# Kernel optimization log

Hardware: AMD Instinct MI355X
Metric: run time of the kernel (lower is better)

The kernel has to match this reference:

```python
import jax, jax.numpy as jnp
import numpy as np

# dims: B batch, T seq, DM d_model, H kv heads, D head dim
B, T, DM = 4, 2048, 768
H, D = 4, 64          # n_kv_heads, d_head = d_model // n_heads = 768 // 12
DIM = H * D           # 256


def setup_inputs() -> dict:
    key = jax.random.key(0)
    kx, kq, kk, kv, ko, kg = jax.random.split(key, 6)
    s = 0.02  # init scale for weights
    return {
        "x": jax.random.normal(kx, (B, T, DM), jnp.float32),
        "Wq": jax.random.normal(kq, (DM, DIM), jnp.float32) * s,
        "Wk": jax.random.normal(kk, (DM, DIM), jnp.float32) * s,
        "Wv": jax.random.normal(kv, (DM, DIM), jnp.float32) * s,
        "Wo": jax.random.normal(ko, (DIM, DM), jnp.float32) * s,
        "Wg": jax.random.normal(kg, (DM, DM), jnp.float32) * s,
    }


def _feature_map(x):
    # F.elu(x) + 1.0  (strictly positive features)
    return jax.nn.elu(x) + 1.0


def reference(x, Wq, Wk, Wv, Wo, Wg):
    Bx, Tx, _ = x.shape
    q = _feature_map((x @ Wq).reshape(Bx, Tx, H, D))
    k = _feature_map((x @ Wk).reshape(Bx, Tx, H, D))
    v = (x @ Wv).reshape(Bx, Tx, H, D)

    # time-major for scan: [T, B, H, D]
    qT = q.transpose(1, 0, 2, 3)
    kT = k.transpose(1, 0, 2, 3)
    vT = v.transpose(1, 0, 2, 3)

    S0 = jnp.zeros((Bx, H, D, D), x.dtype)  # running sum of k v^T
    z0 = jnp.zeros((Bx, H, D), x.dtype)     # running sum of k

    def step(carry, inp):
        S, z = carry
        qi, ki, vi = inp  # each [B, H, D]
        S = S + ki[..., :, None] * vi[..., None, :]   # outer product update
        z = z + ki
        num = jnp.einsum('bhd,bhde->bhe', qi, S)
        den = jnp.maximum(jnp.sum(qi * z, axis=-1), 1e-6)  # clamp(min=1e-6)
        return (S, z), num / den[..., None]

    (_, _), outT = jax.lax.scan(step, (S0, z0), (qT, kT, vT))

    out = outT.transpose(1, 0, 2, 3).reshape(Bx, Tx, DIM)  # [B, T, H*D]
    gate = jax.nn.sigmoid(x @ Wg)
    return (out @ Wo) * gate
```

## Files before the change

kernel.cpp:

```cpp
#include <hip/hip_runtime.h>
#include <math.h>

typedef __attribute__((ext_vector_type(8))) short bf16x8;
typedef __attribute__((ext_vector_type(4))) float f32x4;

namespace {
constexpr int Bb  = 4;
constexpr int Tt  = 2048;
constexpr int DM  = 768;
constexpr int Hh  = 4;
constexpr int Dd  = 64;
constexpr int DIM = 256;
constexpr int BT  = Bb * Tt;
constexpr int CH  = 64;
constexpr int NC  = Tt / CH;
constexpr int NQKVG = 1536;
constexpr int MT  = BT / 128;
}

__device__ __forceinline__ float elu1(float x) { return x > 0.f ? x + 1.f : expf(x); }

__device__ __forceinline__ unsigned short f2bf(float f) {
  unsigned int x = __float_as_uint(f);
  unsigned int r = (x + 0x7fffu + ((x >> 16) & 1u)) >> 16;
  return (unsigned short)r;
}
__device__ __forceinline__ float bf2f(unsigned short u) {
  return __uint_as_float((unsigned int)u << 16);
}

__device__ __forceinline__ void gload16(const void* g, void* l) {
  __builtin_amdgcn_global_load_lds(
      (const __attribute__((address_space(1))) void*)g,
      (__attribute__((address_space(3))) void*)l, 16, 0, 0);
}

struct Stage32 {
  const short* a[2];
  const short* b[2];
  int seg;
  __device__ __forceinline__ void init(const short* Ag, size_t lda,
                                       const short* Bg, size_t ldb, int w, int l) {
    const int c16 = (l & 3) ^ ((l >> 3) & 3);
    seg = w * 2;
#pragma unroll
    for (int j = 0; j < 2; ++j) {
      int row = (seg + j) * 16 + (l >> 2);
      a[j] = Ag + (size_t)row * lda + c16 * 8;
      b[j] = Bg + (size_t)row * ldb + c16 * 8;
    }
  }
  __device__ __forceinline__ void issue(int k0, short* as, short* bs) const {
#pragma unroll
    for (int j = 0; j < 2; ++j) {
      gload16(a[j] + k0, (char*)as + (seg + j) * 1024);
      gload16(b[j] + k0, (char*)bs + (seg + j) * 1024);
    }
  }
};

__device__ __forceinline__ void xcd_tile(int bid, int& mt, int& nt) {
  int xcd = bid & 7;
  int idx = bid >> 3;
  mt = xcd * 8 + (idx & 7);
  nt = idx >> 3;
}

template <int NT>
__device__ __forceinline__ void kloop32(const Stage32& st, short* As0, short* As1,
                                        short* Bs0, short* Bs1,
                                        f32x4 (&acc)[4][4], int wr, int wc,
                                        int lr, int lg) {
  st.issue(0, As0, Bs0);
  st.issue(32, As1, Bs1);
#pragma unroll
  for (int t = 0; t < NT; ++t) {
    short* as = (t & 1) ? As1 : As0;
    short* bs = (t & 1) ? Bs1 : Bs0;
    if (t + 1 < NT)
      asm volatile("s_waitcnt vmcnt(4)" ::: "memory");
    else
      asm volatile("s_waitcnt vmcnt(0)" ::: "memory");
    __builtin_amdgcn_s_barrier();
    bf16x8 af[4], bf[4];
#pragma unroll
    for (int mi = 0; mi < 4; ++mi) {
      int r = wr * 64 + mi * 16 + lr;
      af[mi] = *(const bf16x8*)&as[r * 32 + (lg ^ ((r >> 1) & 3)) * 8];
    }
#pragma unroll
    for (int ni = 0; ni < 4; ++ni) {
      int r = wc * 64 + ni * 16 + lr;
      bf[ni] = *(const bf16x8*)&bs[r * 32 + (lg ^ ((r >> 1) & 3)) * 8];
    }
    asm volatile("s_waitcnt lgkmcnt(0)" ::: "memory");
    __builtin_amdgcn_sched_barrier(0);
    __builtin_amdgcn_s_barrier();
    if (t + 2 < NT) st.issue((t + 2) * 32, as, bs);
    __builtin_amdgcn_s_setprio(1);
#pragma unroll
    for (int mi = 0; mi < 4; ++mi)
#pragma unroll
      for (int ni = 0; ni < 4; ++ni)
        acc[mi][ni] = __builtin_amdgcn_mfma_f32_16x16x32_bf16(
            af[mi], bf[ni], acc[mi][ni], 0, 0, 0);
    __builtin_amdgcn_s_setprio(0);
  }
}

__global__ __launch_bounds__(256) void k_prep(
    const float* __restrict__ x, const float* __restrict__ Wq,
    const float* __restrict__ Wk, const float* __restrict__ Wv,
    const float* __restrict__ Wg, const float* __restrict__ Wo,
    unsigned short* __restrict__ xb, unsigned short* __restrict__ WT,
    unsigned short* __restrict__ WoT) {
  int bid = blockIdx.x;
  if (bid < 3072) {
    int i = bid * 256 + threadIdx.x;
    const float4* p = (const float4*)(x + (size_t)i * 8);
    float4 a = p[0], b = p[1];
    union { unsigned short u[8]; uint4 v; } r;
    r.u[0] = f2bf(a.x); r.u[1] = f2bf(a.y); r.u[2] = f2bf(a.z); r.u[3] = f2bf(a.w);
    r.u[4] = f2bf(b.x); r.u[5] = f2bf(b.y); r.u[6] = f2bf(b.z); r.u[7] = f2bf(b.w);
    *(uint4*)(xb + (size_t)i * 8) = r.v;
    return;
  }
  __shared__ float t[32][33];
  int idx = bid - 3072;
  const float* src;
  unsigned short* out;
  int K, N, n_off, ldo;
  if (idx < 576) {
    int z = idx / 192;
    idx %= 192;
    src = (z == 0) ? Wq : (z == 1) ? Wk : Wv;
    out = WT; K = 768; N = 256; n_off = z * 256; ldo = 768;
  } else if (idx < 1152) {
    idx -= 576;
    src = Wg; out = WT; K = 768; N = 768; n_off = 768; ldo = 768;
  } else {
    idx -= 1152;
    src = Wo; out = WoT; K = 256; N = 768; n_off = 0; ldo = 256;
  }
  int kt = idx % (K / 32), nt = idx / (K / 32);
  int k0 = kt * 32, n0 = nt * 32;
  const int tx = threadIdx.x & 31, ty = threadIdx.x >> 5;
  for (int i = ty; i < 32; i += 8)
    t[i][tx] = src[(size_t)(k0 + i) * N + n0 + tx];
  __syncthreads();
  for (int i = ty; i < 32; i += 8)
    out[(size_t)(n_off + n0 + i) * ldo + k0 + tx] = f2bf(t[tx][i]);
}

__global__ __launch_bounds__(256, 4) void k_gemm1(
    const unsigned short* __restrict__ xb, const unsigned short* __restrict__ WT,
    unsigned short* __restrict__ Q, unsigned short* __restrict__ K,
    unsigned short* __restrict__ V, unsigned short* __restrict__ G) {
  __shared__ __align__(16) char smem[32768];
  short* As0 = (short*)smem;
  short* As1 = (short*)(smem + 8192);
  short* Bs0 = (short*)(smem + 16384);
  short* Bs1 = (short*)(smem + 24576);
  const int tid = threadIdx.x;
  const int w = tid >> 6, l = tid & 63;
  const int lr = l & 15, lg = l >> 4;
  const int wr = w >> 1, wc = w & 1;
  int mt, nt;
  xcd_tile(blockIdx.x, mt, nt);
  const int m0 = mt * 128, n0 = nt * 128;

  Stage32 st;
  st.init((const short*)xb + (size_t)m0 * DM, DM,
          (const short*)WT + (size_t)n0 * DM, DM, w, l);

  f32x4 acc[4][4];
#pragma unroll
  for (int i = 0; i < 4; ++i)
#pragma unroll
    for (int j = 0; j < 4; ++j) acc[i][j] = (f32x4){0.f, 0.f, 0.f, 0.f};

  kloop32<DM / 32>(st, As0, As1, Bs0, Bs1, acc, wr, wc, lr, lg);
  __syncthreads();

  const int ttype = (n0 < 512) ? 0 : (n0 < 768) ? 1 : 2;
  unsigned short* Cs = (unsigned short*)smem;
#pragma unroll
  for (int mi = 0; mi < 4; ++mi)
#pragma unroll
    for (int ni = 0; ni < 4; ++ni)
#pragma unroll
      for (int r = 0; r < 4; ++r) {
        float v = acc[mi][ni][r];
        if (ttype == 0) v = elu1(v);
        else if (ttype == 2) v = 1.f / (1.f + expf(-v));
        Cs[(wr * 64 + mi * 16 + lg * 4 + r) * 128 + wc * 64 + ni * 16 + lr] =
            f2bf(v);
      }
  __syncthreads();
  unsigned short* dst;
  int ldd, cb;
  if (n0 < 256)      { dst = Q; ldd = DIM; cb = n0; }
  else if (n0 < 512) { dst = K; ldd = DIM; cb = n0 - 256; }
  else if (n0 < 768) { dst = V; ldd = DIM; cb = n0 - 512; }
  else               { dst = G; ldd = DM;  cb = n0 - 768; }
  const uint4* Cv = (const uint4*)Cs;
#pragma unroll
  for (int i = 0; i < 8; ++i) {
    int idx = tid + i * 256;
    int urow = idx >> 4, uc = idx & 15;
    *(uint4*)(dst + (size_t)(m0 + urow) * ldd + cb + uc * 8) = Cv[idx];
  }
}

__global__ __launch_bounds__(256) void k_chunksum(
    const unsigned short* __restrict__ K, const unsigned short* __restrict__ V,
    float* __restrict__ Sc, float* __restrict__ zc) {
  __shared__ __align__(16) char smem[16384];
  short* Kt = (short*)smem;
  short* Vt = (short*)(smem + 8192);
  const int c = blockIdx.x, h = blockIdx.y, b = blockIdx.z;
  const int tid = threadIdx.x;
  const int w = tid >> 6, l = tid & 63;
  const int lr = l & 15, lg = l >> 4;
  const size_t rowbase = ((size_t)(b * Tt + c * CH)) * DIM + h * Dd;

#pragma unroll
  for (int it = 0; it < 4; ++it) {
    int idx = tid + it * 256;
    int t = idx >> 4, d4 = idx & 15;
    short4 k4 = *(const short4*)((const short*)K + rowbase + (size_t)t * DIM + d4 * 4);
    short4 v4 = *(const short4*)((const short*)V + rowbase + (size_t)t * DIM + d4 * 4);
    const short* kk = (const short*)&k4;
    const short* vv = (const short*)&v4;
#pragma unroll
    for (int j = 0; j < 4; ++j) {
      int e = d4 * 4 + j;
      int sl = ((t >> 3) ^ (e & 7)) * 16 + (t & 7) * 2;
      *(short*)((char*)Kt + e * 128 + sl) = kk[j];
      *(short*)((char*)Vt + e * 128 + sl) = vv[j];
    }
  }
  __syncthreads();

  if (tid < Dd) {
    float s = 0.f;
    for (int t = 0; t < CH; ++t) {
      unsigned short u = *(const unsigned short*)(
          (char*)Kt + tid * 128 + (((t >> 3) ^ (tid & 7)) * 16) + (t & 7) * 2);
      s += bf2f(u);
    }
    zc[((size_t)(b * Hh + h) * NC + c) * Dd + tid] = s;
  }

  f32x4 a[4];
#pragma unroll
  for (int nf = 0; nf < 4; ++nf) a[nf] = (f32x4){0.f, 0.f, 0.f, 0.f};
  const int rd = w * 16 + lr;
#pragma unroll
  for (int ks = 0; ks < 2; ++ks) {
    bf16x8 af = *(const bf16x8*)((char*)Kt + rd * 128 +
                                 (((ks * 4 + lg) ^ (rd & 7)) * 16));
#pragma unroll
    for (int nf = 0; nf < 4; ++nf) {
      int re = nf * 16 + lr;
      bf16x8 bf = *(const bf16x8*)((char*)Vt + re * 128 +
                                   (((ks * 4 + lg) ^ (re & 7)) * 16));
      a[nf] = __builtin_amdgcn_mfma_f32_16x16x32_bf16(af, bf, a[nf], 0, 0, 0);
    }
  }
  __syncthreads();

  float* Cf = (float*)smem;
#pragma unroll
  for (int nf = 0; nf < 4; ++nf)
#pragma unroll
    for (int r = 0; r < 4; ++r)
      Cf[(w * 16 + lg * 4 + r) * 64 + nf * 16 + lr] = a[nf][r];
  __syncthreads();
  const size_t base = ((size_t)(b * Hh + h) * NC + c) * (Dd * Dd);
  const float4* Cv = (const float4*)Cf;
#pragma unroll
  for (int it = 0; it < 4; ++it) {
    int idx = tid + it * 256;
    *(float4*)&Sc[base + (size_t)idx * 4] = Cv[idx];
  }
}

__global__ __launch_bounds__(256) void k_scan(float* __restrict__ Sc,
                                              float* __restrict__ zc) {
  const int bh = blockIdx.x;
  const int o = blockIdx.y * 256 + threadIdx.x;
  const size_t base = (size_t)bh * NC * (Dd * Dd) + o;
  float v[NC];
#pragma unroll
  for (int c = 0; c < NC; ++c) v[c] = Sc[base + (size_t)c * (Dd * Dd)];
  float run = 0.f;
#pragma unroll
  for (int c = 0; c < NC; ++c) {
    Sc[base + (size_t)c * (Dd * Dd)] = run;
    run += v[c];
  }
  if (blockIdx.y == 0 && threadIdx.x < Dd) {
    float rz = 0.f;
    for (int c = 0; c < NC; ++c) {
      size_t oz = ((size_t)bh * NC + c) * Dd + threadIdx.x;
      float cur = zc[oz];
      zc[oz] = rz;
      rz += cur;
    }
  }
}

__global__ __launch_bounds__(256) void k_out(
    const unsigned short* __restrict__ Q, const unsigned short* __restrict__ K,
    const unsigned short* __restrict__ V, const float* __restrict__ Sc,
    const float* __restrict__ zc, unsigned short* __restrict__ O) {
  __shared__ __align__(16) char smem[41216];
  short* Qs = (short*)smem;
  short* Ks = (short*)(smem + 8192);
  short* Vt = (short*)(smem + 16384);
  short* St = (short*)(smem + 24576);
  short* Ps = (short*)(smem + 32768);
  float* zs = (float*)(smem + 40960);
  const int c = blockIdx.x, h = blockIdx.y, b = blockIdx.z;
  const int tid = threadIdx.x;
  const int w = tid >> 6, l = tid & 63;
  const int lr = l & 15, lg = l >> 4;
  const size_t rowbase = ((size_t)(b * Tt + c * CH)) * DIM + h * Dd;

  {
    const int c16 = (l & 7) ^ ((l >> 3) & 7);
#pragma unroll
    for (int i = 0; i < 2; ++i) {
      int row = i * 32 + w * 8 + (l >> 3);
      gload16((const short*)Q + rowbase + (size_t)row * DIM + c16 * 8,
              (char*)Qs + (i * 32 + w * 8) * 128);
      gload16((const short*)K + rowbase + (size_t)row * DIM + c16 * 8,
              (char*)Ks + (i * 32 + w * 8) * 128);
    }
  }
  const size_t sbase = ((size_t)(b * Hh + h) * NC + c) * (Dd * Dd);
  if (tid < Dd) zs[tid] = zc[((size_t)(b * Hh + h) * NC + c) * Dd + tid];
#pragma unroll
  for (int it = 0; it < 4; ++it) {
    int idx = tid + it * 256;
    int t = idx >> 4, d4 = idx & 15;
    short4 v4 = *(const short4*)((const short*)V + rowbase + (size_t)t * DIM + d4 * 4);
    const short* vv = (const short*)&v4;
#pragma unroll
    for (int j = 0; j < 4; ++j) {
      int e = d4 * 4 + j;
      *(short*)((char*)Vt + e * 128 + (((t >> 3) ^ (e & 7)) * 16) + (t & 7) * 2) = vv[j];
    }
    float4 s4 = *(const float4*)&Sc[sbase + (size_t)t * 64 + d4 * 4];
    const float* sv = (const float*)&s4;
#pragma unroll
    for (int j = 0; j < 4; ++j) {
      int e = d4 * 4 + j;
      *(short*)((char*)St + e * 128 + (((t >> 3) ^ (e & 7)) * 16) + (t & 7) * 2) =
          (short)f2bf(sv[j]);
    }
  }
  __syncthreads();

  f32x4 a0[4];
#pragma unroll
  for (int nf = 0; nf < 4; ++nf) a0[nf] = (f32x4){0.f, 0.f, 0.f, 0.f};
  const int rq = w * 16 + lr;
#pragma unroll
  for (int ks = 0; ks < 2; ++ks) {
    bf16x8 af = *(const bf16x8*)((char*)Qs + rq * 128 +
                                 (((ks * 4 + lg) ^ (rq & 7)) * 16));
#pragma unroll
    for (int nf = 0; nf < 4; ++nf) {
      int rk = nf * 16 + lr;
      bf16x8 bf = *(const bf16x8*)((char*)Ks + rk * 128 +
                                   (((ks * 4 + lg) ^ (rk & 7)) * 16));
      a0[nf] = __builtin_amdgcn_mfma_f32_16x16x32_bf16(af, bf, a0[nf], 0, 0, 0);
    }
  }

  float part[4] = {0.f, 0.f, 0.f, 0.f};
#pragma unroll
  for (int nf = 0; nf < 4; ++nf) {
    int col = nf * 16 + lr;
#pragma unroll
    for (int r = 0; r < 4; ++r) {
      int row = w * 16 + lg * 4 + r;
      float av = (col <= row) ? a0[nf][r] : 0.f;
      part[r] += av;
      *(short*)((char*)Ps + row * 128 +
                ((((nf * 2) + (lr >> 3)) ^ (row & 7)) * 16) + (lr & 7) * 2) =
          (short)f2bf(av);
    }
  }
#pragma unroll
  for (int r = 0; r < 4; ++r) {
    int row = w * 16 + lg * 4 + r;
#pragma unroll
    for (int j = 0; j < 4; ++j) {
      int d = lr + j * 16;
      unsigned short qu = *(const unsigned short*)(
          (char*)Qs + row * 128 + (((d >> 3) ^ (row & 7)) * 16) + (d & 7) * 2);
      part[r] += bf2f(qu) * zs[d];
    }
  }
  float inv[4];
#pragma unroll
  for (int r = 0; r < 4; ++r) {
    float s = part[r];
    s += __shfl_xor(s, 1);
    s += __shfl_xor(s, 2);
    s += __shfl_xor(s, 4);
    s += __shfl_xor(s, 8);
    inv[r] = 1.f / fmaxf(s, 1e-6f);
  }
  __syncthreads();

  f32x4 a1[4];
#pragma unroll
  for (int nf = 0; nf < 4; ++nf) a1[nf] = (f32x4){0.f, 0.f, 0.f, 0.f};
#pragma unroll
  for (int ks = 0; ks < 4; ++ks) {
    const char* abase = (ks < 2) ? (const char*)Ps : (const char*)Qs;
    const char* bbase = (ks < 2) ? (const char*)Vt : (const char*)St;
    int kslot = (ks & 1) * 4 + lg;
    bf16x8 af = *(const bf16x8*)(abase + rq * 128 + ((kslot ^ (rq & 7)) * 16));
#pragma unroll
    for (int nf = 0; nf < 4; ++nf) {
      int re = nf * 16 + lr;
      bf16x8 bf = *(const bf16x8*)(bbase + re * 128 + ((kslot ^ (re & 7)) * 16));
      a1[nf] = __builtin_amdgcn_mfma_f32_16x16x32_bf16(af, bf, a1[nf], 0, 0, 0);
    }
  }
  __syncthreads();

#pragma unroll
  for (int nf = 0; nf < 4; ++nf)
#pragma unroll
    for (int r = 0; r < 4; ++r) {
      int row = w * 16 + lg * 4 + r;
      Ps[row * 64 + nf * 16 + lr] = (short)f2bf(a1[nf][r] * inv[r]);
    }
  __syncthreads();
  const uint4* Pv = (const uint4*)Ps;
#pragma unroll
  for (int i = 0; i < 2; ++i) {
    int idx = tid + i * 256;
    int row = idx >> 3, uc = idx & 7;
    *(uint4*)((unsigned short*)O + rowbase + (size_t)row * DIM + uc * 8) = Pv[idx];
  }
}

__global__ __launch_bounds__(256, 4) void k_gemm2(
    const unsigned short* __restrict__ Ob, const unsigned short* __restrict__ WoT,
    const unsigned short* __restrict__ G, float* __restrict__ out) {
  __shared__ __align__(16) char smem[32768];
  short* As0 = (short*)smem;
  short* As1 = (short*)(smem + 8192);
  short* Bs0 = (short*)(smem + 16384);
  short* Bs1 = (short*)(smem + 24576);
  const int tid = threadIdx.x;
  const int w = tid >> 6, l = tid & 63;
  const int lr = l & 15, lg = l >> 4;
  const int wr = w >> 1, wc = w & 1;
  int mt, nt;
  xcd_tile(blockIdx.x, mt, nt);
  const int m0 = mt * 128, n0 = nt * 128;

  Stage32 st;
  st.init((const short*)Ob + (size_t)m0 * DIM, DIM,
          (const short*)WoT + (size_t)n0 * DIM, DIM, w, l);

  f32x4 acc[4][4];
#pragma unroll
  for (int i = 0; i < 4; ++i)
#pragma unroll
    for (int j = 0; j < 4; ++j) acc[i][j] = (f32x4){0.f, 0.f, 0.f, 0.f};

  kloop32<DIM / 32>(st, As0, As1, Bs0, Bs1, acc, wr, wc, lr, lg);

  float* Cf = (float*)smem;
#pragma unroll
  for (int half = 0; half < 2; ++half) {
    __syncthreads();
    if (wr == half) {
#pragma unroll
      for (int mi = 0; mi < 4; ++mi)
#pragma unroll
        for (int ni = 0; ni < 4; ++ni)
#pragma unroll
          for (int r = 0; r < 4; ++r)
            Cf[(mi * 16 + lg * 4 + r) * 128 + wc * 64 + ni * 16 + lr] =
                acc[mi][ni][r];
    }
    __syncthreads();
    const float4* Cv = (const float4*)Cf;
#pragma unroll
    for (int i = 0; i < 8; ++i) {
      int idx = tid + i * 256;
      int urow = idx >> 5, uc = idx & 31;
      float4 cv = Cv[idx];
      size_t go = (size_t)(m0 + half * 64 + urow) * DM + n0 + uc * 4;
      short4 g4 = *(const short4*)(G + go);
      float4 ov;
      ov.x = cv.x * bf2f(g4.x);
      ov.y = cv.y * bf2f(g4.y);
      ov.z = cv.z * bf2f(g4.z);
      ov.w = cv.w * bf2f(g4.w);
      *(float4*)(out + go) = ov;
    }
  }
}

extern "C" void kernel_launch(void* const* d_in, const int* in_sizes, int n_in,
                              void* d_out, int out_size, void* d_ws,
                              size_t ws_size, hipStream_t stream) {
  const float* x  = (const float*)d_in[0];
  const float* Wq = (const float*)d_in[1];
  const float* Wk = (const float*)d_in[2];
  const float* Wv = (const float*)d_in[3];
  const float* Wo = (const float*)d_in[4];
  const float* Wg = (const float*)d_in[5];
  float* out = (float*)d_out;

  char* p = (char*)d_ws;
  size_t off = 0;
  auto alloc = [&](size_t bytes) {
    void* r = p + off;
    off = (off + bytes + 255) & ~(size_t)255;
    return r;
  };
  unsigned short* xb  = (unsigned short*)alloc((size_t)BT * DM * 2);
  unsigned short* WT  = (unsigned short*)alloc((size_t)NQKVG * DM * 2);
  unsigned short* WoT = (unsigned short*)alloc((size_t)DM * DIM * 2);
  unsigned short* Q   = (unsigned short*)alloc((size_t)BT * DIM * 2);
  unsigned short* Kf  = (unsigned short*)alloc((size_t)BT * DIM * 2);
  unsigned short* Vf  = (unsigned short*)alloc((size_t)BT * DIM * 2);
  unsigned short* G   = (unsigned short*)alloc((size_t)BT * DM * 2);
  unsigned short* Ob  = (unsigned short*)alloc((size_t)BT * DIM * 2);
  float* Sc = (float*)alloc((size_t)Bb * Hh * NC * Dd * Dd * 4);
  float* zc = (float*)alloc((size_t)Bb * Hh * NC * Dd * 4);

  k_prep<<<dim3(3072 + 1344), dim3(256), 0, stream>>>(x, Wq, Wk, Wv, Wg, Wo,
                                                      xb, WT, WoT);

  k_gemm1<<<dim3(MT * (NQKVG / 128)), dim3(256), 0, stream>>>(
      xb, WT, Q, Kf, Vf, G);

  k_chunksum<<<dim3(NC, Hh, Bb), dim3(256), 0, stream>>>(Kf, Vf, Sc, zc);
  k_scan<<<dim3(Bb * Hh, Dd * Dd / 256), dim3(256), 0, stream>>>(Sc, zc);
  k_out<<<dim3(NC, Hh, Bb), dim3(256), 0, stream>>>(Q, Kf, Vf, Sc, zc, Ob);

  k_gemm2<<<dim3(MT * (DM / 128)), dim3(256), 0, stream>>>(Ob, WoT, G, out);
}
```

Baseline: 76.95 us.

## Widen GEMM tiles to 128x256 for projection and output GEMMs

Both bf16 MFMA GEMMs move from 128x128 to 128x256 output tiles. Each warp now computes a 64x128 sub-tile with 32 accumulators, and the B-operand staging and LDS buffers grow to match. The aim is better operand reuse per loaded A tile and fewer blocks. In exchange, register pressure roughly doubles (launch bounds drop to 2 blocks per CU), and grid sizes halve (gemm1 goes to 384 blocks, gemm2 to 192), which may underfill 256 CUs. The epilogues are split into column halves and quarters to fit the shared scratch buffer.

```diff
diff --git a/kernel.cpp b/kernel.cpp
--- a/kernel.cpp
+++ b/kernel.cpp
@@ -35,27 +35,33 @@
       (__attribute__((address_space(3))) void*)l, 16, 0, 0);
 }
 
-struct Stage32 {
+struct StageW {
   const short* a[2];
-  const short* b[2];
-  int seg;
+  const short* b[4];
+  int sega, segb;
   __device__ __forceinline__ void init(const short* Ag, size_t lda,
                                        const short* Bg, size_t ldb, int w, int l) {
     const int c16 = (l & 3) ^ ((l >> 3) & 3);
-    seg = w * 2;
+    sega = w * 2;
+    segb = w * 4;
 #pragma unroll
     for (int j = 0; j < 2; ++j) {
-      int row = (seg + j) * 16 + (l >> 2);
+      int row = (sega + j) * 16 + (l >> 2);
       a[j] = Ag + (size_t)row * lda + c16 * 8;
+    }
+#pragma unroll
+    for (int j = 0; j < 4; ++j) {
+      int row = (segb + j) * 16 + (l >> 2);
       b[j] = Bg + (size_t)row * ldb + c16 * 8;
     }
   }
   __device__ __forceinline__ void issue(int k0, short* as, short* bs) const {
 #pragma unroll
-    for (int j = 0; j < 2; ++j) {
-      gload16(a[j] + k0, (char*)as + (seg + j) * 1024);
-      gload16(b[j] + k0, (char*)bs + (seg + j) * 1024);
-    }
+    for (int j = 0; j < 2; ++j)
+      gload16(a[j] + k0, (char*)as + (sega + j) * 1024);
+#pragma unroll
+    for (int j = 0; j < 4; ++j)
+      gload16(b[j] + k0, (char*)bs + (segb + j) * 1024);
   }
 };
 
@@ -67,10 +73,10 @@
 }
 
 template <int NT>
-__device__ __forceinline__ void kloop32(const Stage32& st, short* As0, short* As1,
-                                        short* Bs0, short* Bs1,
-                                        f32x4 (&acc)[4][4], int wr, int wc,
-                                        int lr, int lg) {
+__device__ __forceinline__ void kloopW(const StageW& st, short* As0, short* As1,
+                                       short* Bs0, short* Bs1,
+                                       f32x4 (&acc)[4][8], int wr, int wc,
+                                       int lr, int lg) {
   st.issue(0, As0, Bs0);
   st.issue(32, As1, Bs1);
 #pragma unroll
@@ -78,19 +84,19 @@
     short* as = (t & 1) ? As1 : As0;
     short* bs = (t & 1) ? Bs1 : Bs0;
     if (t + 1 < NT)
-      asm volatile("s_waitcnt vmcnt(4)" ::: "memory");
+      asm volatile("s_waitcnt vmcnt(6)" ::: "memory");
     else
       asm volatile("s_waitcnt vmcnt(0)" ::: "memory");
     __builtin_amdgcn_s_barrier();
-    bf16x8 af[4], bf[4];
+    bf16x8 af[4], bf[8];
 #pragma unroll
     for (int mi = 0; mi < 4; ++mi) {
       int r = wr * 64 + mi * 16 + lr;
       af[mi] = *(const bf16x8*)&as[r * 32 + (lg ^ ((r >> 1) & 3)) * 8];
     }
 #pragma unroll
-    for (int ni = 0; ni < 4; ++ni) {
-      int r = wc * 64 + ni * 16 + lr;
+    for (int ni = 0; ni < 8; ++ni) {
+      int r = wc * 128 + ni * 16 + lr;
       bf[ni] = *(const bf16x8*)&bs[r * 32 + (lg ^ ((r >> 1) & 3)) * 8];
     }
     asm volatile("s_waitcnt lgkmcnt(0)" ::: "memory");
@@ -101,7 +107,7 @@
 #pragma unroll
     for (int mi = 0; mi < 4; ++mi)
 #pragma unroll
-      for (int ni = 0; ni < 4; ++ni)
+      for (int ni = 0; ni < 8; ++ni)
         acc[mi][ni] = __builtin_amdgcn_mfma_f32_16x16x32_bf16(
             af[mi], bf[ni], acc[mi][ni], 0, 0, 0);
     __builtin_amdgcn_s_setprio(0);
@@ -152,63 +158,68 @@
     out[(size_t)(n_off + n0 + i) * ldo + k0 + tx] = f2bf(t[tx][i]);
 }
 
-__global__ __launch_bounds__(256, 4) void k_gemm1(
+__global__ __launch_bounds__(256, 2) void k_gemm1(
     const unsigned short* __restrict__ xb, const unsigned short* __restrict__ WT,
     unsigned short* __restrict__ Q, unsigned short* __restrict__ K,
     unsigned short* __restrict__ V, unsigned short* __restrict__ G) {
-  __shared__ __align__(16) char smem[32768];
+  __shared__ __align__(16) char smem[49152];
   short* As0 = (short*)smem;
   short* As1 = (short*)(smem + 8192);
   short* Bs0 = (short*)(smem + 16384);
-  short* Bs1 = (short*)(smem + 24576);
+  short* Bs1 = (short*)(smem + 32768);
   const int tid = threadIdx.x;
   const int w = tid >> 6, l = tid & 63;
   const int lr = l & 15, lg = l >> 4;
   const int wr = w >> 1, wc = w & 1;
   int mt, nt;
   xcd_tile(blockIdx.x, mt, nt);
-  const int m0 = mt * 128, n0 = nt * 128;
-
-  Stage32 st;
+  const int m0 = mt * 128, n0 = nt * 256;
+
+  StageW st;
   st.init((const short*)xb + (size_t)m0 * DM, DM,
           (const short*)WT + (size_t)n0 * DM, DM, w, l);
 
-  f32x4 acc[4][4];
+  f32x4 acc[4][8];
 #pragma unroll
   for (int i = 0; i < 4; ++i)
 #pragma unroll
-    for (int j = 0; j < 4; ++j) acc[i][j] = (f32x4){0.f, 0.f, 0.f, 0.f};
-
-  kloop32<DM / 32>(st, As0, As1, Bs0, Bs1, acc, wr, wc, lr, lg);
-  __syncthreads();
+    for (int j = 0; j < 8; ++j) acc[i][j] = (f32x4){0.f, 0.f, 0.f, 0.f};
+
+  kloopW<DM / 32>(st, As0, As1, Bs0, Bs1, acc, wr, wc, lr, lg);
 
   const int ttype = (n0 < 512) ? 0 : (n0 < 768) ? 1 : 2;
-  unsigned short* Cs = (unsigned short*)smem;
-#pragma unroll
-  for (int mi = 0; mi < 4; ++mi)
-#pragma unroll
-    for (int ni = 0; ni < 4; ++ni)
-#pragma unroll
-      for (int r = 0; r < 4; ++r) {
-        float v = acc[mi][ni][r];
-        if (ttype == 0) v = elu1(v);
-        else if (ttype == 2) v = 1.f / (1.f + expf(-v));
-        Cs[(wr * 64 + mi * 16 + lg * 4 + r) * 128 + wc * 64 + ni * 16 + lr] =
-            f2bf(v);
-      }
-  __syncthreads();
   unsigned short* dst;
   int ldd, cb;
-  if (n0 < 256)      { dst = Q; ldd = DIM; cb = n0; }
-  else if (n0 < 512) { dst = K; ldd = DIM; cb = n0 - 256; }
-  else if (n0 < 768) { dst = V; ldd = DIM; cb = n0 - 512; }
+  if (n0 < 256)      { dst = Q; ldd = DIM; cb = 0; }
+  else if (n0 < 512) { dst = K; ldd = DIM; cb = 0; }
+  else if (n0 < 768) { dst = V; ldd = DIM; cb = 0; }
   else               { dst = G; ldd = DM;  cb = n0 - 768; }
-  const uint4* Cv = (const uint4*)Cs;
-#pragma unroll
-  for (int i = 0; i < 8; ++i) {
-    int idx = tid + i * 256;
-    int urow = idx >> 4, uc = idx & 15;
-    *(uint4*)(dst + (size_t)(m0 + urow) * ldd + cb + uc * 8) = Cv[idx];
+  unsigned short* Cs = (unsigned short*)smem;
+#pragma unroll
+  for (int hc = 0; hc < 2; ++hc) {
+    __syncthreads();
+    if (wc == hc) {
+#pragma unroll
+      for (int mi = 0; mi < 4; ++mi)
+#pragma unroll
+        for (int ni = 0; ni < 8; ++ni)
+#pragma unroll
+          for (int r = 0; r < 4; ++r) {
+            float v = acc[mi][ni][r];
+            if (ttype == 0) v = elu1(v);
+            else if (ttype == 2) v = 1.f / (1.f + expf(-v));
+            Cs[(wr * 64 + mi * 16 + lg * 4 + r) * 128 + ni * 16 + lr] = f2bf(v);
+          }
+    }
+    __syncthreads();
+    const uint4* Cv = (const uint4*)Cs;
+#pragma unroll
+    for (int i = 0; i < 8; ++i) {
+      int idx = tid + i * 256;
+      int urow = idx >> 4, uc = idx & 15;
+      *(uint4*)(dst + (size_t)(m0 + urow) * ldd + cb + hc * 128 + uc * 8) =
+          Cv[idx];
+    }
   }
 }
 
@@ -452,65 +463,66 @@
   }
 }
 
-__global__ __launch_bounds__(256, 4) void k_gemm2(
+__global__ __launch_bounds__(256, 2) void k_gemm2(
     const unsigned short* __restrict__ Ob, const unsigned short* __restrict__ WoT,
     const unsigned short* __restrict__ G, float* __restrict__ out) {
-  __shared__ __align__(16) char smem[32768];
+  __shared__ __align__(16) char smem[49152];
   short* As0 = (short*)smem;
   short* As1 = (short*)(smem + 8192);
   short* Bs0 = (short*)(smem + 16384);
-  short* Bs1 = (short*)(smem + 24576);
+  short* Bs1 = (short*)(smem + 32768);
   const int tid = threadIdx.x;
   const int w = tid >> 6, l = tid & 63;
   const int lr = l & 15, lg = l >> 4;
   const int wr = w >> 1, wc = w & 1;
   int mt, nt;
   xcd_tile(blockIdx.x, mt, nt);
-  const int m0 = mt * 128, n0 = nt * 128;
-
-  Stage32 st;
+  const int m0 = mt * 128, n0 = nt * 256;
+
+  StageW st;
   st.init((const short*)Ob + (size_t)m0 * DIM, DIM,
           (const short*)WoT + (size_t)n0 * DIM, DIM, w, l);
 
-  f32x4 acc[4][4];
+  f32x4 acc[4][8];
 #pragma unroll
   for (int i = 0; i < 4; ++i)
 #pragma unroll
-    for (int j = 0; j < 4; ++j) acc[i][j] = (f32x4){0.f, 0.f, 0.f, 0.f};
-
-  kloop32<DIM / 32>(st, As0, As1, Bs0, Bs1, acc, wr, wc, lr, lg);
+    for (int j = 0; j < 8; ++j) acc[i][j] = (f32x4){0.f, 0.f, 0.f, 0.f};
+
+  kloopW<DIM / 32>(st, As0, As1, Bs0, Bs1, acc, wr, wc, lr, lg);
 
   float* Cf = (float*)smem;
 #pragma unroll
-  for (int half = 0; half < 2; ++half) {
-    __syncthreads();
-    if (wr == half) {
-#pragma unroll
-      for (int mi = 0; mi < 4; ++mi)
-#pragma unroll
-        for (int ni = 0; ni < 4; ++ni)
-#pragma unroll
-          for (int r = 0; r < 4; ++r)
-            Cf[(mi * 16 + lg * 4 + r) * 128 + wc * 64 + ni * 16 + lr] =
-                acc[mi][ni][r];
-    }
-    __syncthreads();
-    const float4* Cv = (const float4*)Cf;
-#pragma unroll
-    for (int i = 0; i < 8; ++i) {
-      int idx = tid + i * 256;
-      int urow = idx >> 5, uc = idx & 31;
-      float4 cv = Cv[idx];
-      size_t go = (size_t)(m0 + half * 64 + urow) * DM + n0 + uc * 4;
-      short4 g4 = *(const short4*)(G + go);
-      float4 ov;
-      ov.x = cv.x * bf2f(g4.x);
-      ov.y = cv.y * bf2f(g4.y);
-      ov.z = cv.z * bf2f(g4.z);
-      ov.w = cv.w * bf2f(g4.w);
-      *(float4*)(out + go) = ov;
-    }
-  }
+  for (int qr = 0; qr < 2; ++qr)
+#pragma unroll
+    for (int qc = 0; qc < 2; ++qc) {
+      __syncthreads();
+      if (wr == qr && wc == qc) {
+#pragma unroll
+        for (int mi = 0; mi < 4; ++mi)
+#pragma unroll
+          for (int ni = 0; ni < 8; ++ni)
+#pragma unroll
+            for (int r = 0; r < 4; ++r)
+              Cf[(mi * 16 + lg * 4 + r) * 128 + ni * 16 + lr] = acc[mi][ni][r];
+      }
+      __syncthreads();
+      const float4* Cv = (const float4*)Cf;
+#pragma unroll
+      for (int i = 0; i < 8; ++i) {
+        int idx = tid + i * 256;
+        int urow = idx >> 5, uc = idx & 31;
+        float4 cv = Cv[idx];
+        size_t go = (size_t)(m0 + qr * 64 + urow) * DM + n0 + qc * 128 + uc * 4;
+        short4 g4 = *(const short4*)(G + go);
+        float4 ov;
+        ov.x = cv.x * bf2f(g4.x);
+        ov.y = cv.y * bf2f(g4.y);
+        ov.z = cv.z * bf2f(g4.z);
+        ov.w = cv.w * bf2f(g4.w);
+        *(float4*)(out + go) = ov;
+      }
+    }
 }
 
 extern "C" void kernel_launch(void* const* d_in, const int* in_sizes, int n_in,
@@ -545,12 +557,12 @@
   k_prep<<<dim3(3072 + 1344), dim3(256), 0, stream>>>(x, Wq, Wk, Wv, Wg, Wo,
                                                       xb, WT, WoT);
 
-  k_gemm1<<<dim3(MT * (NQKVG / 128)), dim3(256), 0, stream>>>(
+  k_gemm1<<<dim3(MT * (NQKVG / 256)), dim3(256), 0, stream>>>(
       xb, WT, Q, Kf, Vf, G);
 
   k_chunksum<<<dim3(NC, Hh, Bb), dim3(256), 0, stream>>>(Kf, Vf, Sc, zc);
   k_scan<<<dim3(Bb * Hh, Dd * Dd / 256), dim3(256), 0, stream>>>(Sc, zc);
   k_out<<<dim3(NC, Hh, Bb), dim3(256), 0, stream>>>(Q, Kf, Vf, Sc, zc, Ob);
 
-  k_gemm2<<<dim3(MT * (DM / 128)), dim3(256), 0, stream>>>(Ob, WoT, G, out);
-}
+  k_gemm2<<<dim3(MT * (DM / 256)), dim3(256), 0, stream>>>(Ob, WoT, G, out);
+}
```

After: 95.76 us. +24.4%, slower.

## Triple-buffer GEMM k-loop and store chunk state sums in bf16

Applied to the files above, without the earlier changes.

The GEMM main loop moves from two LDS stages to three. This lets the prefetch for stage t+2 be issued right after the first barrier, and the second per-iteration barrier is removed. LDS per block grows to 48KB and launch bounds drop to 3 blocks per CU. Separately, the per-chunk KV state sums are stored and scanned in bf16 instead of fp32, which halves the traffic through chunksum, scan and out. The cost is extra rounding in the prefix sums, which are carried in fp32 but written back as bf16. The scan also no longer preloads all chunks into registers.

```diff
diff --git a/kernel.cpp b/kernel.cpp
--- a/kernel.cpp
+++ b/kernel.cpp
@@ -67,21 +67,27 @@
 }
 
 template <int NT>
-__device__ __forceinline__ void kloop32(const Stage32& st, short* As0, short* As1,
-                                        short* Bs0, short* Bs1,
-                                        f32x4 (&acc)[4][4], int wr, int wc,
-                                        int lr, int lg) {
-  st.issue(0, As0, Bs0);
-  st.issue(32, As1, Bs1);
+__device__ __forceinline__ void kloop3(const Stage32& st,
+                                       short* A0, short* A1, short* A2,
+                                       short* B0, short* B1, short* B2,
+                                       f32x4 (&acc)[4][4], int wr, int wc,
+                                       int lr, int lg) {
+  st.issue(0, A0, B0);
+  st.issue(32, A1, B1);
 #pragma unroll
   for (int t = 0; t < NT; ++t) {
-    short* as = (t & 1) ? As1 : As0;
-    short* bs = (t & 1) ? Bs1 : Bs0;
+    short* as = ((t % 3) == 0) ? A0 : ((t % 3) == 1) ? A1 : A2;
+    short* bs = ((t % 3) == 0) ? B0 : ((t % 3) == 1) ? B1 : B2;
     if (t + 1 < NT)
       asm volatile("s_waitcnt vmcnt(4)" ::: "memory");
     else
       asm volatile("s_waitcnt vmcnt(0)" ::: "memory");
     __builtin_amdgcn_s_barrier();
+    if (t + 2 < NT) {
+      short* an = (((t + 2) % 3) == 0) ? A0 : (((t + 2) % 3) == 1) ? A1 : A2;
+      short* bn = (((t + 2) % 3) == 0) ? B0 : (((t + 2) % 3) == 1) ? B1 : B2;
+      st.issue((t + 2) * 32, an, bn);
+    }
     bf16x8 af[4], bf[4];
 #pragma unroll
     for (int mi = 0; mi < 4; ++mi) {
@@ -95,8 +101,6 @@
     }
     asm volatile("s_waitcnt lgkmcnt(0)" ::: "memory");
     __builtin_amdgcn_sched_barrier(0);
-    __builtin_amdgcn_s_barrier();
-    if (t + 2 < NT) st.issue((t + 2) * 32, as, bs);
     __builtin_amdgcn_s_setprio(1);
 #pragma unroll
     for (int mi = 0; mi < 4; ++mi)
@@ -152,15 +156,17 @@
     out[(size_t)(n_off + n0 + i) * ldo + k0 + tx] = f2bf(t[tx][i]);
 }
 
-__global__ __launch_bounds__(256, 4) void k_gemm1(
+__global__ __launch_bounds__(256, 3) void k_gemm1(
     const unsigned short* __restrict__ xb, const unsigned short* __restrict__ WT,
     unsigned short* __restrict__ Q, unsigned short* __restrict__ K,
     unsigned short* __restrict__ V, unsigned short* __restrict__ G) {
-  __shared__ __align__(16) char smem[32768];
-  short* As0 = (short*)smem;
-  short* As1 = (short*)(smem + 8192);
-  short* Bs0 = (short*)(smem + 16384);
-  short* Bs1 = (short*)(smem + 24576);
+  __shared__ __align__(16) char smem[49152];
+  short* A0 = (short*)smem;
+  short* A1 = (short*)(smem + 8192);
+  short* A2 = (short*)(smem + 16384);
+  short* B0 = (short*)(smem + 24576);
+  short* B1 = (short*)(smem + 32768);
+  short* B2 = (short*)(smem + 40960);
   const int tid = threadIdx.x;
   const int w = tid >> 6, l = tid & 63;
   const int lr = l & 15, lg = l >> 4;
@@ -179,7 +185,7 @@
 #pragma unroll
     for (int j = 0; j < 4; ++j) acc[i][j] = (f32x4){0.f, 0.f, 0.f, 0.f};
 
-  kloop32<DM / 32>(st, As0, As1, Bs0, Bs1, acc, wr, wc, lr, lg);
+  kloop3<DM / 32>(st, A0, A1, A2, B0, B1, B2, acc, wr, wc, lr, lg);
   __syncthreads();
 
   const int ttype = (n0 < 512) ? 0 : (n0 < 768) ? 1 : 2;
@@ -214,7 +220,7 @@
 
 __global__ __launch_bounds__(256) void k_chunksum(
     const unsigned short* __restrict__ K, const unsigned short* __restrict__ V,
-    float* __restrict__ Sc, float* __restrict__ zc) {
+    unsigned short* __restrict__ Sc, float* __restrict__ zc) {
   __shared__ __align__(16) char smem[16384];
   short* Kt = (short*)smem;
   short* Vt = (short*)(smem + 8192);
@@ -270,35 +276,34 @@
   }
   __syncthreads();
 
-  float* Cf = (float*)smem;
+  unsigned short* Cb = (unsigned short*)smem;
 #pragma unroll
   for (int nf = 0; nf < 4; ++nf)
 #pragma unroll
     for (int r = 0; r < 4; ++r)
-      Cf[(w * 16 + lg * 4 + r) * 64 + nf * 16 + lr] = a[nf][r];
+      Cb[(w * 16 + lg * 4 + r) * 64 + nf * 16 + lr] = f2bf(a[nf][r]);
   __syncthreads();
   const size_t base = ((size_t)(b * Hh + h) * NC + c) * (Dd * Dd);
-  const float4* Cv = (const float4*)Cf;
-#pragma unroll
-  for (int it = 0; it < 4; ++it) {
+  const uint4* Cv = (const uint4*)Cb;
+#pragma unroll
+  for (int it = 0; it < 2; ++it) {
     int idx = tid + it * 256;
-    *(float4*)&Sc[base + (size_t)idx * 4] = Cv[idx];
-  }
-}
-
-__global__ __launch_bounds__(256) void k_scan(float* __restrict__ Sc,
+    *(uint4*)&Sc[base + (size_t)idx * 8] = Cv[idx];
+  }
+}
+
+__global__ __launch_bounds__(256) void k_scan(unsigned short* __restrict__ Sc,
                                               float* __restrict__ zc) {
   const int bh = blockIdx.x;
   const int o = blockIdx.y * 256 + threadIdx.x;
   const size_t base = (size_t)bh * NC * (Dd * Dd) + o;
-  float v[NC];
-#pragma unroll
-  for (int c = 0; c < NC; ++c) v[c] = Sc[base + (size_t)c * (Dd * Dd)];
   float run = 0.f;
 #pragma unroll
   for (int c = 0; c < NC; ++c) {
-    Sc[base + (size_t)c * (Dd * Dd)] = run;
-    run += v[c];
+    size_t off = base + (size_t)c * (Dd * Dd);
+    float cur = bf2f(Sc[off]);
+    Sc[off] = f2bf(run);
+    run += cur;
   }
   if (blockIdx.y == 0 && threadIdx.x < Dd) {
     float rz = 0.f;
@@ -313,7 +318,7 @@
 
 __global__ __launch_bounds__(256) void k_out(
     const unsigned short* __restrict__ Q, const unsigned short* __restrict__ K,
-    const unsigned short* __restrict__ V, const float* __restrict__ Sc,
+    const unsigned short* __restrict__ V, const unsigned short* __restrict__ Sc,
     const float* __restrict__ zc, unsigned short* __restrict__ O) {
   __shared__ __align__(16) char smem[41216];
   short* Qs = (short*)smem;
@@ -352,13 +357,13 @@
       int e = d4 * 4 + j;
       *(short*)((char*)Vt + e * 128 + (((t >> 3) ^ (e & 7)) * 16) + (t & 7) * 2) = vv[j];
     }
-    float4 s4 = *(const float4*)&Sc[sbase + (size_t)t * 64 + d4 * 4];
-    const float* sv = (const float*)&s4;
+    short4 s4 = *(const short4*)((const short*)Sc + sbase + (size_t)t * 64 + d4 * 4);
+    const short* sv = (const short*)&s4;
 #pragma unroll
     for (int j = 0; j < 4; ++j) {
       int e = d4 * 4 + j;
       *(short*)((char*)St + e * 128 + (((t >> 3) ^ (e & 7)) * 16) + (t & 7) * 2) =
-          (short)f2bf(sv[j]);
+          sv[j];
     }
   }
   __syncthreads();
@@ -452,14 +457,16 @@
   }
 }
 
-__global__ __launch_bounds__(256, 4) void k_gemm2(
+__global__ __launch_bounds__(256, 3) void k_gemm2(
     const unsigned short* __restrict__ Ob, const unsigned short* __restrict__ WoT,
     const unsigned short* __restrict__ G, float* __restrict__ out) {
-  __shared__ __align__(16) char smem[32768];
-  short* As0 = (short*)smem;
-  short* As1 = (short*)(smem + 8192);
-  short* Bs0 = (short*)(smem + 16384);
-  short* Bs1 = (short*)(smem + 24576);
+  __shared__ __align__(16) char smem[49152];
+  short* A0 = (short*)smem;
+  short* A1 = (short*)(smem + 8192);
+  short* A2 = (short*)(smem + 16384);
+  short* B0 = (short*)(smem + 24576);
+  short* B1 = (short*)(smem + 32768);
+  short* B2 = (short*)(smem + 40960);
   const int tid = threadIdx.x;
   const int w = tid >> 6, l = tid & 63;
   const int lr = l & 15, lg = l >> 4;
@@ -478,7 +485,7 @@
 #pragma unroll
     for (int j = 0; j < 4; ++j) acc[i][j] = (f32x4){0.f, 0.f, 0.f, 0.f};
 
-  kloop32<DIM / 32>(st, As0, As1, Bs0, Bs1, acc, wr, wc, lr, lg);
+  kloop3<DIM / 32>(st, A0, A1, A2, B0, B1, B2, acc, wr, wc, lr, lg);
 
   float* Cf = (float*)smem;
 #pragma unroll
@@ -539,7 +546,7 @@
   unsigned short* Vf  = (unsigned short*)alloc((size_t)BT * DIM * 2);
   unsigned short* G   = (unsigned short*)alloc((size_t)BT * DM * 2);
   unsigned short* Ob  = (unsigned short*)alloc((size_t)BT * DIM * 2);
-  float* Sc = (float*)alloc((size_t)Bb * Hh * NC * Dd * Dd * 4);
+  unsigned short* Sc  = (unsigned short*)alloc((size_t)Bb * Hh * NC * Dd * Dd * 2);
   float* zc = (float*)alloc((size_t)Bb * Hh * NC * Dd * 4);
 
   k_prep<<<dim3(3072 + 1344), dim3(256), 0, stream>>>(x, Wq, Wk, Wv, Wg, Wo,
```

Result: faster. 74.94 us (-2.6%).
